# Optimization experiments

Measured on AMD Instinct MI355X. Metric: run time of the kernel, lower is better.

The kernel has to match this reference:

```python
import jax, jax.numpy as jnp
import numpy as np

B, S, D, H = 8, 2048, 1024, 16
A = D // H  # attn_dim = 64
SCALE = float(np.sqrt(D))  # module divides by sqrt(d_model), NOT sqrt(attn_dim)


def setup_inputs() -> dict:
    key = jax.random.key(0)
    ks = jax.random.split(key, 6)
    # xavier-uniform bound for Linear(dim -> attn_dim)
    bound = float(np.sqrt(6.0 / (D + A)))
    return {
        "query": jax.random.normal(ks[0], (B, S, D), dtype=jnp.float32),
        "key": jax.random.normal(ks[1], (B, S, D), dtype=jnp.float32),
        "value": jax.random.normal(ks[2], (B, S, D), dtype=jnp.float32),
        "Wq": jax.random.uniform(ks[3], (D, A), jnp.float32, -bound, bound),
        "bq": jnp.zeros((A,), jnp.float32),
        "Wk": jax.random.uniform(ks[4], (D, A), jnp.float32, -bound, bound),
        "bk": jnp.zeros((A,), jnp.float32),
        "Wv": jax.random.uniform(ks[5], (D, A), jnp.float32, -bound, bound),
        "bv": jnp.zeros((A,), jnp.float32),
    }


def reference(query, key, value, Wq, bq, Wk, bk, Wv, bv):
    # Linear projections dim -> attn_dim
    q = query @ Wq + bq  # [B, S, A]
    k = key @ Wk + bk    # [B, S, A]
    v = value @ Wv + bv  # [B, S, A]
    # scaled dot-product attention; score matrix [B, S, S] is materialized
    score = jnp.einsum("bqa,bka->bqk", q, k) / SCALE
    attn = jax.nn.softmax(score, axis=-1)
    # dropout is identity in eval mode
    context = jnp.einsum("bqk,bka->bqa", attn, v)  # [B, S, A]
    return (context, attn)
```

## Files before the change

### kernel.cpp

```cpp
#include <hip/hip_runtime.h>
#include <hip/hip_bf16.h>

#define NB 8
#define SEQ 2048
#define DM 1024
#define AD 64
#define NROWS (NB * SEQ)

#define SCL2 0.04508422f

typedef __attribute__((ext_vector_type(8))) short short8;
typedef __attribute__((ext_vector_type(4))) float f32x4;

static __device__ __forceinline__ unsigned short f2bf(float f) {
    unsigned int u = __float_as_uint(f);
    u += 0x7FFFu + ((u >> 16) & 1u);
    return (unsigned short)(u >> 16);
}

static __device__ __forceinline__ f32x4 mfma16(short8 a, short8 b, f32x4 c) {
    return __builtin_amdgcn_mfma_f32_16x16x32_bf16(a, b, c, 0, 0, 0);
}

static __device__ __forceinline__ short8 pack8v(f32x4 a, f32x4 b) {
    short8 r;
    r[0] = (short)f2bf(a[0]); r[1] = (short)f2bf(a[1]);
    r[2] = (short)f2bf(a[2]); r[3] = (short)f2bf(a[3]);
    r[4] = (short)f2bf(b[0]); r[5] = (short)f2bf(b[1]);
    r[6] = (short)f2bf(b[2]); r[7] = (short)f2bf(b[3]);
    return r;
}

__global__ __launch_bounds__(256) void wT_kernel(
    const float* __restrict__ Wq, const float* __restrict__ Wk,
    const float* __restrict__ Wv, unsigned short* __restrict__ wT) {
    int p = blockIdx.y;
    int k0 = blockIdx.x * 64;
    const float* W = (p == 0) ? Wq : (p == 1) ? Wk : Wv;
    __shared__ unsigned short tl[64][72];
    int t = threadIdx.x;
    int c = t & 63;
    int r0 = t >> 6;
    for (int i = 0; i < 16; i++) {
        int k = r0 + i * 4;
        tl[c][k] = f2bf(W[(size_t)(k0 + k) * AD + c]);
    }
    __syncthreads();
    for (int i = 0; i < 16; i++) {
        int a = r0 + i * 4;
        wT[((size_t)p * AD + a) * DM + k0 + c] = tl[a][c];
    }
}

__global__ __launch_bounds__(256, 2) void proj_kernel(
    const float* __restrict__ q_in, const float* __restrict__ k_in,
    const float* __restrict__ v_in, const float* __restrict__ bq,
    const float* __restrict__ bk, const float* __restrict__ bv,
    const unsigned short* __restrict__ wT,
    unsigned short* __restrict__ q_out, unsigned short* __restrict__ k_out,
    unsigned short* __restrict__ vT_out) {
    int p = blockIdx.y;
    int rbase = blockIdx.x * 64;
    const float* X = (p == 0) ? q_in : (p == 1) ? k_in : v_in;
    const float* bias = (p == 0) ? bq : (p == 1) ? bk : bv;
    const unsigned short* wTp = wT + (size_t)p * AD * DM;

    __shared__ float xs[2][64][68];
    __shared__ unsigned short wsm[2][64][72];

    int t = threadIdx.x;
    int lane = t & 63;
    int w = t >> 6;
    int arow = lane & 15;
    int agrp = lane >> 4;

    int srow = t >> 4;
    int scol = (t & 15) * 4;
    int wrow = t >> 2;
    int wcol = (t & 3) * 16;

    const float* Xb = X + (size_t)rbase * DM;

    f32x4 acc[4];
#pragma unroll
    for (int ct = 0; ct < 4; ct++) acc[ct] = (f32x4){0.f, 0.f, 0.f, 0.f};

    float4 px0, px1, px2, px3;
    float4 pw0, pw1;

    px0 = *reinterpret_cast<const float4*>(&Xb[(size_t)(0 * 16 + srow) * DM + scol]);
    px1 = *reinterpret_cast<const float4*>(&Xb[(size_t)(1 * 16 + srow) * DM + scol]);
    px2 = *reinterpret_cast<const float4*>(&Xb[(size_t)(2 * 16 + srow) * DM + scol]);
    px3 = *reinterpret_cast<const float4*>(&Xb[(size_t)(3 * 16 + srow) * DM + scol]);
    {
        const char* wp = reinterpret_cast<const char*>(wTp + (size_t)wrow * DM + wcol);
        pw0 = *reinterpret_cast<const float4*>(wp);
        pw1 = *reinterpret_cast<const float4*>(wp + 16);
    }
    *reinterpret_cast<float4*>(&xs[0][0 * 16 + srow][scol]) = px0;
    *reinterpret_cast<float4*>(&xs[0][1 * 16 + srow][scol]) = px1;
    *reinterpret_cast<float4*>(&xs[0][2 * 16 + srow][scol]) = px2;
    *reinterpret_cast<float4*>(&xs[0][3 * 16 + srow][scol]) = px3;
    *reinterpret_cast<float4*>(&wsm[0][wrow][wcol]) = pw0;
    *reinterpret_cast<float4*>(&wsm[0][wrow][wcol + 8]) = pw1;
    __syncthreads();

    for (int c = 0; c < 16; ++c) {
        int bu = c & 1;
        if (c < 15) {
            int kb = (c + 1) * 64;
            px0 = *reinterpret_cast<const float4*>(&Xb[(size_t)(0 * 16 + srow) * DM + kb + scol]);
            px1 = *reinterpret_cast<const float4*>(&Xb[(size_t)(1 * 16 + srow) * DM + kb + scol]);
            px2 = *reinterpret_cast<const float4*>(&Xb[(size_t)(2 * 16 + srow) * DM + kb + scol]);
            px3 = *reinterpret_cast<const float4*>(&Xb[(size_t)(3 * 16 + srow) * DM + kb + scol]);
            const char* wp = reinterpret_cast<const char*>(wTp + (size_t)wrow * DM + kb + wcol);
            pw0 = *reinterpret_cast<const float4*>(wp);
            pw1 = *reinterpret_cast<const float4*>(wp + 16);
        }
        const float* xr = &xs[bu][w * 16 + arow][0];
#pragma unroll
        for (int s = 0; s < 2; ++s) {
            f32x4 a0 = *reinterpret_cast<const f32x4*>(&xr[s * 32 + agrp * 8]);
            f32x4 a1 = *reinterpret_cast<const f32x4*>(&xr[s * 32 + agrp * 8 + 4]);
            short8 af = pack8v(a0, a1);
#pragma unroll
            for (int ct = 0; ct < 4; ++ct) {
                short8 bf = *reinterpret_cast<const short8*>(
                    &wsm[bu][ct * 16 + arow][s * 32 + agrp * 8]);
                acc[ct] = mfma16(af, bf, acc[ct]);
            }
        }
        if (c < 15) {
            int bo = bu ^ 1;
            *reinterpret_cast<float4*>(&xs[bo][0 * 16 + srow][scol]) = px0;
            *reinterpret_cast<float4*>(&xs[bo][1 * 16 + srow][scol]) = px1;
            *reinterpret_cast<float4*>(&xs[bo][2 * 16 + srow][scol]) = px2;
            *reinterpret_cast<float4*>(&xs[bo][3 * 16 + srow][scol]) = px3;
            *reinterpret_cast<float4*>(&wsm[bo][wrow][wcol]) = pw0;
            *reinterpret_cast<float4*>(&wsm[bo][wrow][wcol + 8]) = pw1;
        }
        __syncthreads();
    }

    if (p < 2) {
        unsigned short* outp = (p == 0) ? q_out : k_out;
#pragma unroll
        for (int ct = 0; ct < 4; ct++) {
            int a = ct * 16 + arow;
            float bv_ = bias[a];
#pragma unroll
            for (int rr = 0; rr < 4; rr++) {
                int row = rbase + w * 16 + agrp * 4 + rr;
                outp[(size_t)row * AD + a] = f2bf(acc[ct][rr] + bv_);
            }
        }
    } else {
        unsigned short* sc = (unsigned short*)&xs[0][0][0];
#pragma unroll
        for (int ct = 0; ct < 4; ct++) {
            int a = ct * 16 + arow;
            float bv_ = bias[a];
#pragma unroll
            for (int rr = 0; rr < 4; rr++) {
                int row = w * 16 + agrp * 4 + rr;
                sc[a * 72 + row] = f2bf(acc[ct][rr] + bv_);
            }
        }
        __syncthreads();
        int bidx = rbase >> 11;
        int sbase = rbase & 2047;
        int rr = t & 63;
        for (int i = 0; i < 16; i++) {
            int a = (t >> 6) + i * 4;
            vT_out[((size_t)bidx * AD + a) * SEQ + sbase + rr] = sc[a * 72 + rr];
        }
    }
}

__global__ __launch_bounds__(128, 6) void sum_kernel(
    const unsigned short* __restrict__ qb, const unsigned short* __restrict__ kb,
    float* __restrict__ rowsumpart) {
    int blk = blockIdx.x;
    int b = blk & 7;
    int sp = (blk >> 3) & 3;
    int qbase = (blk >> 5) * 32;

    __shared__ float wsum[2][32];

    int t = threadIdx.x;
    int lane = t & 63;
    int w = t >> 6;
    int arow = lane & 15;
    int agrp = lane >> 4;

    const unsigned short* qrow = qb + ((size_t)b * SEQ + qbase) * AD;
    short8 qf0a = *reinterpret_cast<const short8*>(qrow + (size_t)arow * AD + agrp * 8);
    short8 qf1a = *reinterpret_cast<const short8*>(qrow + (size_t)arow * AD + 32 + agrp * 8);
    short8 qf0b = *reinterpret_cast<const short8*>(qrow + (size_t)(16 + arow) * AD + agrp * 8);
    short8 qf1b = *reinterpret_cast<const short8*>(qrow + (size_t)(16 + arow) * AD + 32 + agrp * 8);
    const unsigned short* kbp = kb + (size_t)b * SEQ * AD;

    int keybase = sp * 512 + w * 256;
    float sA[4] = {0.f, 0.f, 0.f, 0.f};
    float sB[4] = {0.f, 0.f, 0.f, 0.f};
    for (int kt = 0; kt < 16; ++kt) {
        int key0 = keybase + kt * 16;
        const unsigned short* krow = kbp + (size_t)(key0 + arow) * AD;
        short8 kf0 = *reinterpret_cast<const short8*>(krow + agrp * 8);
        short8 kf1 = *reinterpret_cast<const short8*>(krow + 32 + agrp * 8);
        f32x4 aA = (f32x4){0.f, 0.f, 0.f, 0.f};
        aA = mfma16(qf0a, kf0, aA);
        aA = mfma16(qf1a, kf1, aA);
        f32x4 aB = (f32x4){0.f, 0.f, 0.f, 0.f};
        aB = mfma16(qf0b, kf0, aB);
        aB = mfma16(qf1b, kf1, aB);
#pragma unroll
        for (int r = 0; r < 4; r++) {
            sA[r] += __builtin_amdgcn_exp2f(aA[r] * SCL2);
            sB[r] += __builtin_amdgcn_exp2f(aB[r] * SCL2);
        }
    }
#pragma unroll
    for (int r = 0; r < 4; r++) {
#pragma unroll
        for (int off = 1; off < 16; off <<= 1) {
            sA[r] += __shfl_xor(sA[r], off);
            sB[r] += __shfl_xor(sB[r], off);
        }
    }
    if (arow == 0) {
#pragma unroll
        for (int r = 0; r < 4; r++) {
            wsum[w][agrp * 4 + r] = sA[r];
            wsum[w][16 + agrp * 4 + r] = sB[r];
        }
    }
    __syncthreads();
    if (t < 32)
        rowsumpart[(size_t)sp * NROWS + (size_t)b * SEQ + qbase + t] =
            wsum[0][t] + wsum[1][t];
}

__global__ __launch_bounds__(256) void lr_kernel(
    const float* __restrict__ part, float* __restrict__ lr_g) {
    int i = blockIdx.x * 256 + threadIdx.x;
    float S = part[i] + part[NROWS + i] + part[2 * NROWS + i] + part[3 * NROWS + i];
    lr_g[i] = -__builtin_amdgcn_logf(S);
}

__global__ __launch_bounds__(512, 2) void attn2_kernel(
    const unsigned short* __restrict__ qb, const unsigned short* __restrict__ kb,
    const unsigned short* __restrict__ vT, const float* __restrict__ lr_g,
    float* __restrict__ attn_out, float* __restrict__ ctx_out) {
    int blk = blockIdx.x;
    int b = blk & 7;
    int qbase = (blk >> 3) * 32;

    __shared__ float sf[8][32][68];
    __shared__ float lr_lds[32];

    int t = threadIdx.x;
    int lane = t & 63;
    int w = t >> 6;
    int arow = lane & 15;
    int agrp = lane >> 4;

    if (t < 32) lr_lds[t] = lr_g[(size_t)b * SEQ + qbase + t];

    const unsigned short* qrow = qb + ((size_t)b * SEQ + qbase) * AD;
    short8 qf0a = *reinterpret_cast<const short8*>(qrow + (size_t)arow * AD + agrp * 8);
    short8 qf1a = *reinterpret_cast<const short8*>(qrow + (size_t)arow * AD + 32 + agrp * 8);
    short8 qf0b = *reinterpret_cast<const short8*>(qrow + (size_t)(16 + arow) * AD + agrp * 8);
    short8 qf1b = *reinterpret_cast<const short8*>(qrow + (size_t)(16 + arow) * AD + 32 + agrp * 8);
    const unsigned short* kbp = kb + (size_t)b * SEQ * AD;
    const unsigned short* vTb = vT + (size_t)b * AD * SEQ;
    float* attn_b = attn_out + ((size_t)b * SEQ + qbase) * SEQ;
    __syncthreads();

    float lrA[4], lrB[4];
#pragma unroll
    for (int r = 0; r < 4; r++) {
        lrA[r] = lr_lds[agrp * 4 + r];
        lrB[r] = lr_lds[16 + agrp * 4 + r];
    }

    f32x4 caccA[4], caccB[4];
#pragma unroll
    for (int ct = 0; ct < 4; ct++) {
        caccA[ct] = (f32x4){0.f, 0.f, 0.f, 0.f};
        caccB[ct] = (f32x4){0.f, 0.f, 0.f, 0.f};
    }

    int keybase = w * 256;
    for (int g = 0; g < 4; ++g) {
        int key0b = keybase + g * 64;
#pragma unroll
        for (int kb4 = 0; kb4 < 4; ++kb4) {
            int k0 = key0b + kb4 * 16;
            const unsigned short* krow = kbp + (size_t)(k0 + arow) * AD;
            short8 kf0 = *reinterpret_cast<const short8*>(krow + agrp * 8);
            short8 kf1 = *reinterpret_cast<const short8*>(krow + 32 + agrp * 8);
            f32x4 aA = (f32x4){0.f, 0.f, 0.f, 0.f};
            aA = mfma16(qf0a, kf0, aA);
            aA = mfma16(qf1a, kf1, aA);
            f32x4 aB = (f32x4){0.f, 0.f, 0.f, 0.f};
            aB = mfma16(qf0b, kf0, aB);
            aB = mfma16(qf1b, kf1, aB);
#pragma unroll
            for (int r = 0; r < 4; r++) {
                sf[w][agrp * 4 + r][kb4 * 16 + arow] =
                    __builtin_amdgcn_exp2f(aA[r] * SCL2 + lrA[r]);
                sf[w][16 + agrp * 4 + r][kb4 * 16 + arow] =
                    __builtin_amdgcn_exp2f(aB[r] * SCL2 + lrB[r]);
            }
        }
#pragma unroll
        for (int j = 0; j < 8; ++j) {
            int row = j * 4 + agrp;
            int c4 = arow * 4;
            f32x4 vv = *reinterpret_cast<const f32x4*>(&sf[w][row][c4]);
            __builtin_nontemporal_store(
                vv, reinterpret_cast<f32x4*>(&attn_b[(size_t)row * SEQ + key0b + c4]));
        }
#pragma unroll
        for (int ks = 0; ks < 2; ++ks) {
            f32x4 pa0 = *reinterpret_cast<const f32x4*>(&sf[w][arow][ks * 32 + agrp * 8]);
            f32x4 pa1 = *reinterpret_cast<const f32x4*>(&sf[w][arow][ks * 32 + agrp * 8 + 4]);
            short8 pfA = pack8v(pa0, pa1);
            f32x4 pb0 = *reinterpret_cast<const f32x4*>(&sf[w][16 + arow][ks * 32 + agrp * 8]);
            f32x4 pb1 = *reinterpret_cast<const f32x4*>(&sf[w][16 + arow][ks * 32 + agrp * 8 + 4]);
            short8 pfB = pack8v(pb0, pb1);
#pragma unroll
            for (int ct = 0; ct < 4; ct++) {
                const unsigned short* vr =
                    vTb + (size_t)(ct * 16 + arow) * SEQ + key0b + ks * 32 + agrp * 8;
                short8 vv = *reinterpret_cast<const short8*>(vr);
                caccA[ct] = mfma16(pfA, vv, caccA[ct]);
                caccB[ct] = mfma16(pfB, vv, caccB[ct]);
            }
        }
    }

    __syncthreads();
#pragma unroll
    for (int ct = 0; ct < 4; ct++)
#pragma unroll
        for (int r = 0; r < 4; r++) {
            sf[w][agrp * 4 + r][ct * 16 + arow] = caccA[ct][r];
            sf[w][16 + agrp * 4 + r][ct * 16 + arow] = caccB[ct][r];
        }
    __syncthreads();

    float* ctx_b = ctx_out + ((size_t)b * SEQ + qbase) * AD;
    for (int i = t; i < 32 * 64; i += 512) {
        int r = i >> 6, a = i & 63;
        float v = ((sf[0][r][a] + sf[1][r][a]) + (sf[2][r][a] + sf[3][r][a])) +
                  ((sf[4][r][a] + sf[5][r][a]) + (sf[6][r][a] + sf[7][r][a]));
        __builtin_nontemporal_store(v, &ctx_b[(size_t)r * AD + a]);
    }
}

extern "C" void kernel_launch(void* const* d_in, const int* in_sizes, int n_in,
                              void* d_out, int out_size, void* d_ws, size_t ws_size,
                              hipStream_t stream) {
    const float* q_in = (const float*)d_in[0];
    const float* k_in = (const float*)d_in[1];
    const float* v_in = (const float*)d_in[2];
    const float* Wq = (const float*)d_in[3];
    const float* bq = (const float*)d_in[4];
    const float* Wk = (const float*)d_in[5];
    const float* bk = (const float*)d_in[6];
    const float* Wv = (const float*)d_in[7];
    const float* bv = (const float*)d_in[8];

    char* ws = (char*)d_ws;
    unsigned short* q_bf = (unsigned short*)(ws);
    unsigned short* k_bf = (unsigned short*)(ws + (2u << 20));
    unsigned short* vT   = (unsigned short*)(ws + (4u << 20));
    unsigned short* wT   = (unsigned short*)(ws + (6u << 20));
    float* rowsumpart    = (float*)(ws + (7u << 20));
    float* lr_g          = (float*)(ws + (7u << 20) + (256u << 10));

    float* ctx_out = (float*)d_out;
    float* attn_out = ctx_out + (size_t)NB * SEQ * AD;

    hipLaunchKernelGGL(wT_kernel, dim3(16, 3), dim3(256), 0, stream, Wq, Wk, Wv, wT);
    hipLaunchKernelGGL(proj_kernel, dim3(256, 3), dim3(256), 0, stream,
                       q_in, k_in, v_in, bq, bk, bv, wT, q_bf, k_bf, vT);
    hipLaunchKernelGGL(sum_kernel, dim3(2048), dim3(128), 0, stream,
                       q_bf, k_bf, rowsumpart);
    hipLaunchKernelGGL(lr_kernel, dim3(64), dim3(256), 0, stream, rowsumpart, lr_g);
    hipLaunchKernelGGL(attn2_kernel, dim3(512), dim3(512), 0, stream,
                       q_bf, k_bf, vT, lr_g, attn_out, ctx_out);
}
```

Baseline: 107.5 us.

## Give each wave private X staging and read weights from global in projection

Result: slower. 128.9 us (+19.9%).

```diff
diff --git a/kernel.cpp b/kernel.cpp
--- a/kernel.cpp
+++ b/kernel.cpp
@@ -52,7 +52,7 @@
     }
 }
 
-__global__ __launch_bounds__(256, 2) void proj_kernel(
+__global__ __launch_bounds__(256, 4) void proj_kernel(
     const float* __restrict__ q_in, const float* __restrict__ k_in,
     const float* __restrict__ v_in, const float* __restrict__ bq,
     const float* __restrict__ bk, const float* __restrict__ bv,
@@ -65,8 +65,7 @@
     const float* bias = (p == 0) ? bq : (p == 1) ? bk : bv;
     const unsigned short* wTp = wT + (size_t)p * AD * DM;
 
-    __shared__ float xs[2][64][68];
-    __shared__ unsigned short wsm[2][64][72];
+    __shared__ float xs[4][2][16][68];
 
     int t = threadIdx.x;
     int lane = t & 63;
@@ -74,72 +73,59 @@
     int arow = lane & 15;
     int agrp = lane >> 4;
 
-    int srow = t >> 4;
-    int scol = (t & 15) * 4;
-    int wrow = t >> 2;
-    int wcol = (t & 3) * 16;
-
-    const float* Xb = X + (size_t)rbase * DM;
+    int sr = lane >> 4;
+    int sc = (lane & 15) * 4;
+
+    const float* Xw = X + (size_t)(rbase + w * 16) * DM;
+    float (*xsw)[16][68] = xs[w];
 
     f32x4 acc[4];
 #pragma unroll
     for (int ct = 0; ct < 4; ct++) acc[ct] = (f32x4){0.f, 0.f, 0.f, 0.f};
 
-    float4 px0, px1, px2, px3;
-    float4 pw0, pw1;
-
-    px0 = *reinterpret_cast<const float4*>(&Xb[(size_t)(0 * 16 + srow) * DM + scol]);
-    px1 = *reinterpret_cast<const float4*>(&Xb[(size_t)(1 * 16 + srow) * DM + scol]);
-    px2 = *reinterpret_cast<const float4*>(&Xb[(size_t)(2 * 16 + srow) * DM + scol]);
-    px3 = *reinterpret_cast<const float4*>(&Xb[(size_t)(3 * 16 + srow) * DM + scol]);
-    {
-        const char* wp = reinterpret_cast<const char*>(wTp + (size_t)wrow * DM + wcol);
-        pw0 = *reinterpret_cast<const float4*>(wp);
-        pw1 = *reinterpret_cast<const float4*>(wp + 16);
-    }
-    *reinterpret_cast<float4*>(&xs[0][0 * 16 + srow][scol]) = px0;
-    *reinterpret_cast<float4*>(&xs[0][1 * 16 + srow][scol]) = px1;
-    *reinterpret_cast<float4*>(&xs[0][2 * 16 + srow][scol]) = px2;
-    *reinterpret_cast<float4*>(&xs[0][3 * 16 + srow][scol]) = px3;
-    *reinterpret_cast<float4*>(&wsm[0][wrow][wcol]) = pw0;
-    *reinterpret_cast<float4*>(&wsm[0][wrow][wcol + 8]) = pw1;
-    __syncthreads();
+    float4 st0, st1, st2, st3;
+
+    st0 = *reinterpret_cast<const float4*>(&Xw[(size_t)(sr + 0) * DM + sc]);
+    st1 = *reinterpret_cast<const float4*>(&Xw[(size_t)(sr + 4) * DM + sc]);
+    st2 = *reinterpret_cast<const float4*>(&Xw[(size_t)(sr + 8) * DM + sc]);
+    st3 = *reinterpret_cast<const float4*>(&Xw[(size_t)(sr + 12) * DM + sc]);
+    *reinterpret_cast<float4*>(&xsw[0][sr + 0][sc]) = st0;
+    *reinterpret_cast<float4*>(&xsw[0][sr + 4][sc]) = st1;
+    *reinterpret_cast<float4*>(&xsw[0][sr + 8][sc]) = st2;
+    *reinterpret_cast<float4*>(&xsw[0][sr + 12][sc]) = st3;
 
     for (int c = 0; c < 16; ++c) {
         int bu = c & 1;
         if (c < 15) {
-            int kb = (c + 1) * 64;
-            px0 = *reinterpret_cast<const float4*>(&Xb[(size_t)(0 * 16 + srow) * DM + kb + scol]);
-            px1 = *reinterpret_cast<const float4*>(&Xb[(size_t)(1 * 16 + srow) * DM + kb + scol]);
-            px2 = *reinterpret_cast<const float4*>(&Xb[(size_t)(2 * 16 + srow) * DM + kb + scol]);
-            px3 = *reinterpret_cast<const float4*>(&Xb[(size_t)(3 * 16 + srow) * DM + kb + scol]);
-            const char* wp = reinterpret_cast<const char*>(wTp + (size_t)wrow * DM + kb + wcol);
-            pw0 = *reinterpret_cast<const float4*>(wp);
-            pw1 = *reinterpret_cast<const float4*>(wp + 16);
-        }
-        const float* xr = &xs[bu][w * 16 + arow][0];
-#pragma unroll
-        for (int s = 0; s < 2; ++s) {
-            f32x4 a0 = *reinterpret_cast<const f32x4*>(&xr[s * 32 + agrp * 8]);
-            f32x4 a1 = *reinterpret_cast<const f32x4*>(&xr[s * 32 + agrp * 8 + 4]);
-            short8 af = pack8v(a0, a1);
-#pragma unroll
-            for (int ct = 0; ct < 4; ++ct) {
-                short8 bf = *reinterpret_cast<const short8*>(
-                    &wsm[bu][ct * 16 + arow][s * 32 + agrp * 8]);
-                acc[ct] = mfma16(af, bf, acc[ct]);
-            }
+            const float* Xn = Xw + (c + 1) * 64;
+            st0 = *reinterpret_cast<const float4*>(&Xn[(size_t)(sr + 0) * DM + sc]);
+            st1 = *reinterpret_cast<const float4*>(&Xn[(size_t)(sr + 4) * DM + sc]);
+            st2 = *reinterpret_cast<const float4*>(&Xn[(size_t)(sr + 8) * DM + sc]);
+            st3 = *reinterpret_cast<const float4*>(&Xn[(size_t)(sr + 12) * DM + sc]);
+        }
+        const float* xr = &xsw[bu][arow][0];
+        f32x4 a0 = *reinterpret_cast<const f32x4*>(&xr[agrp * 8]);
+        f32x4 a1 = *reinterpret_cast<const f32x4*>(&xr[agrp * 8 + 4]);
+        short8 af0 = pack8v(a0, a1);
+        f32x4 a2 = *reinterpret_cast<const f32x4*>(&xr[32 + agrp * 8]);
+        f32x4 a3 = *reinterpret_cast<const f32x4*>(&xr[32 + agrp * 8 + 4]);
+        short8 af1 = pack8v(a2, a3);
+        int kb = c * 64;
+#pragma unroll
+        for (int ct = 0; ct < 4; ct++) {
+            const unsigned short* wr = wTp + (size_t)(ct * 16 + arow) * DM + kb;
+            short8 bf0 = *reinterpret_cast<const short8*>(wr + agrp * 8);
+            short8 bf1 = *reinterpret_cast<const short8*>(wr + 32 + agrp * 8);
+            acc[ct] = mfma16(af0, bf0, acc[ct]);
+            acc[ct] = mfma16(af1, bf1, acc[ct]);
         }
         if (c < 15) {
             int bo = bu ^ 1;
-            *reinterpret_cast<float4*>(&xs[bo][0 * 16 + srow][scol]) = px0;
-            *reinterpret_cast<float4*>(&xs[bo][1 * 16 + srow][scol]) = px1;
-            *reinterpret_cast<float4*>(&xs[bo][2 * 16 + srow][scol]) = px2;
-            *reinterpret_cast<float4*>(&xs[bo][3 * 16 + srow][scol]) = px3;
-            *reinterpret_cast<float4*>(&wsm[bo][wrow][wcol]) = pw0;
-            *reinterpret_cast<float4*>(&wsm[bo][wrow][wcol + 8]) = pw1;
-        }
-        __syncthreads();
+            *reinterpret_cast<float4*>(&xsw[bo][sr + 0][sc]) = st0;
+            *reinterpret_cast<float4*>(&xsw[bo][sr + 4][sc]) = st1;
+            *reinterpret_cast<float4*>(&xsw[bo][sr + 8][sc]) = st2;
+            *reinterpret_cast<float4*>(&xsw[bo][sr + 12][sc]) = st3;
+        }
     }
 
     if (p < 2) {
@@ -155,7 +141,8 @@
             }
         }
     } else {
-        unsigned short* sc = (unsigned short*)&xs[0][0][0];
+        __syncthreads();
+        unsigned short* sct = (unsigned short*)&xs[0][0][0][0];
 #pragma unroll
         for (int ct = 0; ct < 4; ct++) {
             int a = ct * 16 + arow;
@@ -163,7 +150,7 @@
 #pragma unroll
             for (int rr = 0; rr < 4; rr++) {
                 int row = w * 16 + agrp * 4 + rr;
-                sc[a * 72 + row] = f2bf(acc[ct][rr] + bv_);
+                sct[a * 72 + row] = f2bf(acc[ct][rr] + bv_);
             }
         }
         __syncthreads();
@@ -172,7 +159,7 @@
         int rr = t & 63;
         for (int i = 0; i < 16; i++) {
             int a = (t >> 6) + i * 4;
-            vT_out[((size_t)bidx * AD + a) * SEQ + sbase + rr] = sc[a * 72 + rr];
+            vT_out[((size_t)bidx * AD + a) * SEQ + sbase + rr] = sct[a * 72 + rr];
         }
     }
 }
```

## Fuse softmax row-sum pass into attention kernel, drop separate sum/log kernels

Applied to the files above, without the earlier changes.

Result: faster. 101.2 us (-5.9%).

```diff
diff --git a/kernel.cpp b/kernel.cpp
--- a/kernel.cpp
+++ b/kernel.cpp
@@ -177,15 +177,17 @@
     }
 }
 
-__global__ __launch_bounds__(128, 6) void sum_kernel(
+__global__ __launch_bounds__(512, 2) void attn2_kernel(
     const unsigned short* __restrict__ qb, const unsigned short* __restrict__ kb,
-    float* __restrict__ rowsumpart) {
+    const unsigned short* __restrict__ vT, float* __restrict__ attn_out,
+    float* __restrict__ ctx_out) {
     int blk = blockIdx.x;
     int b = blk & 7;
-    int sp = (blk >> 3) & 3;
-    int qbase = (blk >> 5) * 32;
-
-    __shared__ float wsum[2][32];
+    int qbase = (blk >> 3) * 32;
+
+    __shared__ float sf[8][32][68];
+    __shared__ float wsum[8][32];
+    __shared__ float lr_lds[32];
 
     int t = threadIdx.x;
     int lane = t & 63;
@@ -199,8 +201,11 @@
     short8 qf0b = *reinterpret_cast<const short8*>(qrow + (size_t)(16 + arow) * AD + agrp * 8);
     short8 qf1b = *reinterpret_cast<const short8*>(qrow + (size_t)(16 + arow) * AD + 32 + agrp * 8);
     const unsigned short* kbp = kb + (size_t)b * SEQ * AD;
-
-    int keybase = sp * 512 + w * 256;
+    const unsigned short* vTb = vT + (size_t)b * AD * SEQ;
+    float* attn_b = attn_out + ((size_t)b * SEQ + qbase) * SEQ;
+
+    int keybase = w * 256;
+
     float sA[4] = {0.f, 0.f, 0.f, 0.f};
     float sB[4] = {0.f, 0.f, 0.f, 0.f};
     for (int kt = 0; kt < 16; ++kt) {
@@ -236,45 +241,11 @@
         }
     }
     __syncthreads();
-    if (t < 32)
-        rowsumpart[(size_t)sp * NROWS + (size_t)b * SEQ + qbase + t] =
-            wsum[0][t] + wsum[1][t];
-}
-
-__global__ __launch_bounds__(256) void lr_kernel(
-    const float* __restrict__ part, float* __restrict__ lr_g) {
-    int i = blockIdx.x * 256 + threadIdx.x;
-    float S = part[i] + part[NROWS + i] + part[2 * NROWS + i] + part[3 * NROWS + i];
-    lr_g[i] = -__builtin_amdgcn_logf(S);
-}
-
-__global__ __launch_bounds__(512, 2) void attn2_kernel(
-    const unsigned short* __restrict__ qb, const unsigned short* __restrict__ kb,
-    const unsigned short* __restrict__ vT, const float* __restrict__ lr_g,
-    float* __restrict__ attn_out, float* __restrict__ ctx_out) {
-    int blk = blockIdx.x;
-    int b = blk & 7;
-    int qbase = (blk >> 3) * 32;
-
-    __shared__ float sf[8][32][68];
-    __shared__ float lr_lds[32];
-
-    int t = threadIdx.x;
-    int lane = t & 63;
-    int w = t >> 6;
-    int arow = lane & 15;
-    int agrp = lane >> 4;
-
-    if (t < 32) lr_lds[t] = lr_g[(size_t)b * SEQ + qbase + t];
-
-    const unsigned short* qrow = qb + ((size_t)b * SEQ + qbase) * AD;
-    short8 qf0a = *reinterpret_cast<const short8*>(qrow + (size_t)arow * AD + agrp * 8);
-    short8 qf1a = *reinterpret_cast<const short8*>(qrow + (size_t)arow * AD + 32 + agrp * 8);
-    short8 qf0b = *reinterpret_cast<const short8*>(qrow + (size_t)(16 + arow) * AD + agrp * 8);
-    short8 qf1b = *reinterpret_cast<const short8*>(qrow + (size_t)(16 + arow) * AD + 32 + agrp * 8);
-    const unsigned short* kbp = kb + (size_t)b * SEQ * AD;
-    const unsigned short* vTb = vT + (size_t)b * AD * SEQ;
-    float* attn_b = attn_out + ((size_t)b * SEQ + qbase) * SEQ;
+    if (t < 32) {
+        float S = ((wsum[0][t] + wsum[1][t]) + (wsum[2][t] + wsum[3][t])) +
+                  ((wsum[4][t] + wsum[5][t]) + (wsum[6][t] + wsum[7][t]));
+        lr_lds[t] = -__builtin_amdgcn_logf(S);
+    }
     __syncthreads();
 
     float lrA[4], lrB[4];
@@ -291,7 +262,6 @@
         caccB[ct] = (f32x4){0.f, 0.f, 0.f, 0.f};
     }
 
-    int keybase = w * 256;
     for (int g = 0; g < 4; ++g) {
         int key0b = keybase + g * 64;
 #pragma unroll
@@ -378,8 +348,6 @@
     unsigned short* k_bf = (unsigned short*)(ws + (2u << 20));
     unsigned short* vT   = (unsigned short*)(ws + (4u << 20));
     unsigned short* wT   = (unsigned short*)(ws + (6u << 20));
-    float* rowsumpart    = (float*)(ws + (7u << 20));
-    float* lr_g          = (float*)(ws + (7u << 20) + (256u << 10));
 
     float* ctx_out = (float*)d_out;
     float* attn_out = ctx_out + (size_t)NB * SEQ * AD;
@@ -387,9 +355,6 @@
     hipLaunchKernelGGL(wT_kernel, dim3(16, 3), dim3(256), 0, stream, Wq, Wk, Wv, wT);
     hipLaunchKernelGGL(proj_kernel, dim3(256, 3), dim3(256), 0, stream,
                        q_in, k_in, v_in, bq, bk, bv, wT, q_bf, k_bf, vT);
-    hipLaunchKernelGGL(sum_kernel, dim3(2048), dim3(128), 0, stream,
-                       q_bf, k_bf, rowsumpart);
-    hipLaunchKernelGGL(lr_kernel, dim3(64), dim3(256), 0, stream, rowsumpart, lr_g);
     hipLaunchKernelGGL(attn2_kernel, dim3(512), dim3(512), 0, stream,
-                       q_bf, k_bf, vT, lr_g, attn_out, ctx_out);
-}
+                       q_bf, k_bf, vT, attn_out, ctx_out);
+}
```
